# Optimization experiments

Hardware: AMD Instinct MI355X
Metric: run time of the kernel (lower is better)

## Reference

```python
import jax, jax.numpy as jnp
import numpy as np

D = 1024
H = 16
HD = D // H


def setup_inputs() -> dict:
    key = jax.random.key(0)
    ks = jax.random.split(key, 12)
    s = 0.02
    return {
        "X": jax.random.normal(ks[0], (8, 1024, D), dtype=jnp.float32),
        "W_qkv": jax.random.normal(ks[1], (D, 3 * D), dtype=jnp.float32) * s,
        "b_qkv": jnp.zeros((3 * D,), dtype=jnp.float32),
        "W_out": jax.random.normal(ks[2], (D, D), dtype=jnp.float32) * s,
        "b_out": jnp.zeros((D,), dtype=jnp.float32),
        "ln1_g": jnp.ones((D,), dtype=jnp.float32),
        "ln1_b": jnp.zeros((D,), dtype=jnp.float32),
        "ln2_g": jnp.ones((D,), dtype=jnp.float32),
        "ln2_b": jnp.zeros((D,), dtype=jnp.float32),
        "W_ff1": jax.random.normal(ks[3], (D, 4 * D), dtype=jnp.float32) * s,
        "b_ff1": jnp.zeros((4 * D,), dtype=jnp.float32),
        "W_ff2": jax.random.normal(ks[4], (4 * D, D), dtype=jnp.float32) * s,
        "b_ff2": jnp.zeros((D,), dtype=jnp.float32),
    }


def _layer_norm(x, g, b, eps=1e-5):
    mu = jnp.mean(x, axis=-1, keepdims=True)
    var = jnp.var(x, axis=-1, keepdims=True)
    return (x - mu) * jax.lax.rsqrt(var + eps) * g + b


def reference(X, W_qkv, b_qkv, W_out, b_out, ln1_g, ln1_b, ln2_g, ln2_b,
              W_ff1, b_ff1, W_ff2, b_ff2):
    B, T, _ = X.shape
    qkv = X @ W_qkv + b_qkv                      # [B,T,3D]
    qkv = qkv.reshape(B, T, 3, H, HD).transpose(2, 0, 3, 1, 4)  # [3,B,H,T,hd]
    Q, K, V = qkv[0], qkv[1], qkv[2]
    scores = jnp.einsum("bhqd,bhkd->bhqk", Q, K) / np.sqrt(HD).astype(np.float32)
    attn = jax.nn.softmax(scores, axis=-1)
    ctx = jnp.einsum("bhqk,bhkd->bhqd", attn, V)  # [B,H,T,hd]
    ctx = ctx.transpose(0, 2, 1, 3).reshape(B, T, D)
    attn_out = ctx @ W_out + b_out
    X1 = _layer_norm(attn_out + X, ln1_g, ln1_b)
    ffn = jax.nn.gelu(X1 @ W_ff1 + b_ff1, approximate=False) @ W_ff2 + b_ff2
    return _layer_norm(ffn + X1, ln2_g, ln2_b)
```

## Files before the change

kernel.cpp:

```cpp
#include <hip/hip_runtime.h>
#include <hip/hip_bf16.h>
#include <cstdint>

typedef unsigned short u16;
typedef __bf16 bf16x8 __attribute__((ext_vector_type(8)));
typedef float f32x4 __attribute__((ext_vector_type(4)));

__device__ __forceinline__ u16 f2bf(float f) {
  unsigned int u = __float_as_uint(f);
  u += 0x7FFFu + ((u >> 16) & 1u);
  return (u16)(u >> 16);
}
__device__ __forceinline__ unsigned int pack2(float a, float b) {
  return (unsigned int)f2bf(a) | ((unsigned int)f2bf(b) << 16);
}

__global__ __launch_bounds__(256) void cast_bf16_k(const float* __restrict__ in,
                                                   u16* __restrict__ out) {
  const int i = (blockIdx.x * 256 + threadIdx.x) * 4;
  const float4 v = *(const float4*)(in + i);
  uint2 p;
  p.x = pack2(v.x, v.y);
  p.y = pack2(v.z, v.w);
  *(uint2*)(out + i) = p;
}

__global__ __launch_bounds__(256) void transpose_cast_k(const float* __restrict__ in,
                                                        u16* __restrict__ out,
                                                        int R, int C) {
  __shared__ float tile[32][33];
  const int bx = blockIdx.x * 32, by = blockIdx.y * 32;
  const int tx = threadIdx.x & 31, ty = threadIdx.x >> 5;
#pragma unroll
  for (int i = 0; i < 32; i += 8)
    tile[ty + i][tx] = in[(size_t)(by + ty + i) * C + (bx + tx)];
  __syncthreads();
#pragma unroll
  for (int i = 0; i < 32; i += 8)
    out[(size_t)(bx + ty + i) * R + (by + tx)] = f2bf(tile[tx][ty + i]);
}

template <int EPI>
__device__ __forceinline__ void epi_store(float v, int row, int col, int N,
                                          const float* __restrict__ resid,
                                          float* __restrict__ out_f,
                                          u16* __restrict__ out_b,
                                          u16* __restrict__ q_out,
                                          u16* __restrict__ k_out,
                                          u16* __restrict__ vt_out) {
  if (EPI == 0) {
    const int which = col >> 10, rem = col & 1023;
    const int h = rem >> 6, d = rem & 63;
    const int b = row >> 10, tq = row & 1023;
    const size_t bh = (size_t)(b * 16 + h);
    const u16 u = f2bf(v);
    if (which == 0)
      q_out[(bh * 1024 + tq) * 64 + d] = u;
    else if (which == 1)
      k_out[(bh * 1024 + tq) * 64 + d] = u;
    else
      vt_out[(bh * 64 + d) * 1024 + tq] = u;
  } else if (EPI == 1) {
    out_f[(size_t)row * N + col] = v + resid[(size_t)row * N + col];
  } else {
    const float gl = 0.5f * v * (1.0f + erff(v * 0.70710678118f));
    out_b[(size_t)row * N + col] = f2bf(gl);
  }
}

#define SYNC_PRE                                      \
  __builtin_amdgcn_s_barrier();                       \
  asm volatile("s_waitcnt lgkmcnt(0)" ::: "memory");  \
  __builtin_amdgcn_sched_barrier(0);                  \
  __builtin_amdgcn_s_setprio(1);

#define SYNC_POST                                     \
  __builtin_amdgcn_s_setprio(0);                      \
  __builtin_amdgcn_sched_barrier(0);                  \
  __builtin_amdgcn_s_barrier();

template <int EPI>
__global__ __launch_bounds__(512, 2) void gemm8(
    const u16* __restrict__ A, const u16* __restrict__ Bt,
    const float* __restrict__ bias, const float* __restrict__ resid,
    float* __restrict__ out_f, u16* __restrict__ out_b,
    u16* __restrict__ q_out, u16* __restrict__ k_out, u16* __restrict__ vt_out,
    int M, int N, int K) {
  __shared__ char lds[131072];
  const int tid = threadIdx.x;
  const int wave = tid >> 6, lane = tid & 63;
  const int llo = lane & 15, lhi = lane >> 4;
  const int wm = wave >> 2, wn = wave & 3;
  const int NT = K >> 6;
  const int nbx = N >> 8;
  const int cpx = gridDim.x >> 3;
  const int wg = (blockIdx.x & 7) * cpx + (blockIdx.x >> 3);
  const int m0 = (wg / nbx) << 8, n0 = (wg % nbx) << 8;

  const int rloc = tid >> 3;
  const int scol = (((tid & 7) * 16) ^ ((rloc & 7) << 4)) >> 1;
  const int swz = (llo & 7) << 4;

  f32x4 acc[8][4] = {};
  bf16x8 aF[2][4][2], bF[2][2][2];

#define STAGE_A(tt, hi)                                                         \
  if ((tt) < NT) {                                                              \
    char* db_ = lds + (((tt) & 1) << 16);                                       \
    _Pragma("unroll") for (int c_ = 0; c_ < 2; ++c_) {                          \
      const u16* g_ =                                                           \
          A + (size_t)(m0 + (hi) * 128 + c_ * 64 + rloc) * K + (tt) * 64 + scol;\
      __builtin_amdgcn_global_load_lds(                                         \
          (const __attribute__((address_space(1))) unsigned int*)g_,            \
          (__attribute__((address_space(3))) unsigned int*)(db_ + (hi) * 16384 +\
                                                           c_ * 8192 + wave * 1024), \
          16, 0, 0);                                                            \
    }                                                                           \
  }

#define STAGE_B(tt, hi)                                                         \
  if ((tt) < NT) {                                                              \
    char* db_ = lds + (((tt) & 1) << 16) + 32768;                               \
    _Pragma("unroll") for (int c_ = 0; c_ < 2; ++c_) {                          \
      const u16* g_ =                                                           \
          Bt + (size_t)(n0 + (hi) * 128 + c_ * 64 + rloc) * K + (tt) * 64 + scol;\
      __builtin_amdgcn_global_load_lds(                                         \
          (const __attribute__((address_space(1))) unsigned int*)g_,            \
          (__attribute__((address_space(3))) unsigned int*)(db_ + (hi) * 16384 +\
                                                           c_ * 8192 + wave * 1024), \
          16, 0, 0);                                                            \
    }                                                                           \
  }

#define LOAD_A(mh)                                                              \
  _Pragma("unroll") for (int mq_ = 0; mq_ < 4; ++mq_)                           \
  _Pragma("unroll") for (int kk_ = 0; kk_ < 2; ++kk_)                           \
    aF[mh][mq_][kk_] = *(const bf16x8*)(ldsA + (wm * 128 + (mh) * 64 + mq_ * 16 + llo) * 128 + \
                                        ((kk_ * 64 + lhi * 16) ^ swz));

#define LOAD_B(nh)                                                              \
  _Pragma("unroll") for (int nf_ = 0; nf_ < 2; ++nf_)                           \
  _Pragma("unroll") for (int kk_ = 0; kk_ < 2; ++kk_)                           \
    bF[nh][nf_][kk_] = *(const bf16x8*)(ldsB + (wn * 64 + (nh) * 32 + nf_ * 16 + llo) * 128 + \
                                        ((kk_ * 64 + lhi * 16) ^ swz));

#define DO_MFMA(mh, nh)                                                         \
  _Pragma("unroll") for (int mq_ = 0; mq_ < 4; ++mq_)                           \
  _Pragma("unroll") for (int nf_ = 0; nf_ < 2; ++nf_)                           \
  _Pragma("unroll") for (int kk_ = 0; kk_ < 2; ++kk_)                           \
    acc[(mh) * 4 + mq_][(nh) * 2 + nf_] = __builtin_amdgcn_mfma_f32_16x16x32_bf16( \
        aF[mh][mq_][kk_], bF[nh][nf_][kk_], acc[(mh) * 4 + mq_][(nh) * 2 + nf_], 0, 0, 0);

  STAGE_A(0, 0) STAGE_A(0, 1) STAGE_B(0, 0) STAGE_B(0, 1) STAGE_A(1, 0) STAGE_A(1, 1)
  asm volatile("s_waitcnt vmcnt(4)" ::: "memory");
  __builtin_amdgcn_s_barrier();

  for (int t = 0; t < NT; ++t) {
    const char* ldsA = lds + ((t & 1) << 16);
    const char* ldsB = ldsA + 32768;
    LOAD_A(0) LOAD_B(0)
    STAGE_B(t + 1, 0)
    SYNC_PRE DO_MFMA(0, 0) SYNC_POST
    LOAD_A(1)
    STAGE_B(t + 1, 1)
    SYNC_PRE DO_MFMA(1, 0) SYNC_POST
    LOAD_B(1)
    STAGE_A(t + 2, 0)
    SYNC_PRE DO_MFMA(0, 1) SYNC_POST
    STAGE_A(t + 2, 1)
    asm volatile("s_waitcnt vmcnt(4)" ::: "memory");
    SYNC_PRE DO_MFMA(1, 1) SYNC_POST
  }

#pragma unroll
  for (int mf = 0; mf < 8; ++mf) {
#pragma unroll
    for (int nf = 0; nf < 4; ++nf) {
      const int col = n0 + wn * 64 + nf * 16 + llo;
      const int rowb = m0 + wm * 128 + mf * 16 + lhi * 4;
      const float bv = bias[col];
#pragma unroll
      for (int r = 0; r < 4; ++r)
        epi_store<EPI>(acc[mf][nf][r] + bv, rowb + r, col, N, resid, out_f, out_b,
                       q_out, k_out, vt_out);
    }
  }
#undef STAGE_A
#undef STAGE_B
#undef LOAD_A
#undef LOAD_B
#undef DO_MFMA
}

template <int EPI>
__global__ __launch_bounds__(512, 2) void gemm8n(
    const u16* __restrict__ A, const u16* __restrict__ Bt,
    const float* __restrict__ bias, const float* __restrict__ resid,
    float* __restrict__ out_f, u16* __restrict__ out_b,
    u16* __restrict__ q_out, u16* __restrict__ k_out, u16* __restrict__ vt_out,
    int M, int N, int K) {
  __shared__ char lds[98304];
  const int tid = threadIdx.x;
  const int wave = tid >> 6, lane = tid & 63;
  const int llo = lane & 15, lhi = lane >> 4;
  const int wm = wave >> 1, wn = wave & 1;
  const int NT = K >> 6;
  const int nbx = N >> 7;
  const int cpx = gridDim.x >> 3;
  const int wg = (blockIdx.x & 7) * cpx + (blockIdx.x >> 3);
  const int m0 = (wg / nbx) << 8, n0 = (wg % nbx) << 7;

  const int rloc = tid >> 3;
  const int scol = (((tid & 7) * 16) ^ ((rloc & 7) << 4)) >> 1;
  const int swz = (llo & 7) << 4;

  f32x4 acc[4][4] = {};
  bf16x8 aF[2][2][2], bF[2][2][2];

#define STAGE_A(tt, hi)                                                         \
  if ((tt) < NT) {                                                              \
    char* db_ = lds + ((tt) & 1) * 49152;                                       \
    _Pragma("unroll") for (int c_ = 0; c_ < 2; ++c_) {                          \
      const u16* g_ =                                                           \
          A + (size_t)(m0 + (hi) * 128 + c_ * 64 + rloc) * K + (tt) * 64 + scol;\
      __builtin_amdgcn_global_load_lds(                                         \
          (const __attribute__((address_space(1))) unsigned int*)g_,            \
          (__attribute__((address_space(3))) unsigned int*)(db_ + (hi) * 16384 +\
                                                           c_ * 8192 + wave * 1024), \
          16, 0, 0);                                                            \
    }                                                                           \
  }

#define STAGE_B(tt)                                                             \
  if ((tt) < NT) {                                                              \
    char* db_ = lds + ((tt) & 1) * 49152 + 32768;                               \
    _Pragma("unroll") for (int c_ = 0; c_ < 2; ++c_) {                          \
      const u16* g_ =                                                           \
          Bt + (size_t)(n0 + c_ * 64 + rloc) * K + (tt) * 64 + scol;            \
      __builtin_amdgcn_global_load_lds(                                         \
          (const __attribute__((address_space(1))) unsigned int*)g_,            \
          (__attribute__((address_space(3))) unsigned int*)(db_ +               \
                                                           c_ * 8192 + wave * 1024), \
          16, 0, 0);                                                            \
    }                                                                           \
  }

#define LOAD_A(mh)                                                              \
  _Pragma("unroll") for (int mf_ = 0; mf_ < 2; ++mf_)                           \
  _Pragma("unroll") for (int kk_ = 0; kk_ < 2; ++kk_)                           \
    aF[mh][mf_][kk_] = *(const bf16x8*)(ldsA + (wm * 64 + (mh) * 32 + mf_ * 16 + llo) * 128 + \
                                        ((kk_ * 64 + lhi * 16) ^ swz));

#define LOAD_B(nh)                                                              \
  _Pragma("unroll") for (int nf_ = 0; nf_ < 2; ++nf_)                           \
  _Pragma("unroll") for (int kk_ = 0; kk_ < 2; ++kk_)                           \
    bF[nh][nf_][kk_] = *(const bf16x8*)(ldsB + (wn * 64 + (nh) * 32 + nf_ * 16 + llo) * 128 + \
                                        ((kk_ * 64 + lhi * 16) ^ swz));

#define DO_MFMA(mh, nh)                                                         \
  _Pragma("unroll") for (int mf_ = 0; mf_ < 2; ++mf_)                           \
  _Pragma("unroll") for (int nf_ = 0; nf_ < 2; ++nf_)                           \
  _Pragma("unroll") for (int kk_ = 0; kk_ < 2; ++kk_)                           \
    acc[(mh) * 2 + mf_][(nh) * 2 + nf_] = __builtin_amdgcn_mfma_f32_16x16x32_bf16( \
        aF[mh][mf_][kk_], bF[nh][nf_][kk_], acc[(mh) * 2 + mf_][(nh) * 2 + nf_], 0, 0, 0);

  STAGE_A(0, 0) STAGE_A(0, 1) STAGE_B(0) STAGE_A(1, 0) STAGE_A(1, 1)
  asm volatile("s_waitcnt vmcnt(4)" ::: "memory");
  __builtin_amdgcn_s_barrier();

  for (int t = 0; t < NT; ++t) {
    const char* ldsA = lds + (t & 1) * 49152;
    const char* ldsB = ldsA + 32768;
    LOAD_A(0) LOAD_B(0)
    STAGE_B(t + 1)
    SYNC_PRE DO_MFMA(0, 0) SYNC_POST
    LOAD_A(1)
    STAGE_A(t + 2, 0)
    SYNC_PRE DO_MFMA(1, 0) SYNC_POST
    LOAD_B(1)
    STAGE_A(t + 2, 1)
    SYNC_PRE DO_MFMA(0, 1) SYNC_POST
    asm volatile("s_waitcnt vmcnt(4)" ::: "memory");
    SYNC_PRE DO_MFMA(1, 1) SYNC_POST
  }

#pragma unroll
  for (int mf = 0; mf < 4; ++mf) {
#pragma unroll
    for (int nf = 0; nf < 4; ++nf) {
      const int col = n0 + wn * 64 + nf * 16 + llo;
      const int rowb = m0 + wm * 64 + mf * 16 + lhi * 4;
      const float bv = bias[col];
#pragma unroll
      for (int r = 0; r < 4; ++r)
        epi_store<EPI>(acc[mf][nf][r] + bv, rowb + r, col, N, resid, out_f, out_b,
                       q_out, k_out, vt_out);
    }
  }
#undef STAGE_A
#undef STAGE_B
#undef LOAD_A
#undef LOAD_B
#undef DO_MFMA
}

__global__ __launch_bounds__(256) void attn_flash_k(const u16* __restrict__ Qb,
                                                    const u16* __restrict__ Kb,
                                                    const u16* __restrict__ Vt,
                                                    u16* __restrict__ ctx) {
  __shared__ char lds[8192 + 8192 + 4 * 2048];
  char* Ks = lds;
  char* Vs = lds + 8192;
  const int tid = threadIdx.x;
  const int wave = tid >> 6, lane = tid & 63;
  const int llo = lane & 15, lhi = lane >> 4;
  char* Ps = lds + 16384 + wave * 2048;
  const int bh = blockIdx.y;
  const int q0 = blockIdx.x * 64 + wave * 16;
  const size_t hq = (size_t)bh * 1024 * 64;
  const int swz = (llo & 7) << 4;

  const u16* qrow = Qb + hq + (size_t)(q0 + llo) * 64;
  const bf16x8 qf0 = *(const bf16x8*)(qrow + lhi * 8);
  const bf16x8 qf1 = *(const bf16x8*)(qrow + 32 + lhi * 8);

  f32x4 O[4] = {};
  float m = -3.0e38f, l = 0.f;
  const float C = 0.18033688011112042f;

  for (int t = 0; t < 16; ++t) {
    const int kv0 = t * 64;
    __syncthreads();
#pragma unroll
    for (int j = 0; j < 2; ++j) {
      const int p = (j * 256 + tid) * 16;
      const int r = p >> 7;
      const int c = (p & 127) ^ ((r & 7) << 4);
      const u16* gk = Kb + hq + (size_t)(kv0 + r) * 64 + (c >> 1);
      __builtin_amdgcn_global_load_lds(
          (const __attribute__((address_space(1))) unsigned int*)gk,
          (__attribute__((address_space(3))) unsigned int*)(Ks + (j * 256 + wave * 64) * 16),
          16, 0, 0);
      const u16* gv = Vt + (size_t)bh * 64 * 1024 + (size_t)r * 1024 + kv0 + (c >> 1);
      __builtin_amdgcn_global_load_lds(
          (const __attribute__((address_space(1))) unsigned int*)gv,
          (__attribute__((address_space(3))) unsigned int*)(Vs + (j * 256 + wave * 64) * 16),
          16, 0, 0);
    }
    __syncthreads();

    f32x4 s[4];
#pragma unroll
    for (int kt = 0; kt < 4; ++kt) {
      const int row = kt * 16 + llo;
      const bf16x8 k0 = *(const bf16x8*)(Ks + row * 128 + ((lhi * 16) ^ swz));
      const bf16x8 k1 = *(const bf16x8*)(Ks + row * 128 + ((64 + lhi * 16) ^ swz));
      f32x4 a = {};
      a = __builtin_amdgcn_mfma_f32_16x16x32_bf16(k0, qf0, a, 0, 0, 0);
      a = __builtin_amdgcn_mfma_f32_16x16x32_bf16(k1, qf1, a, 0, 0, 0);
      s[kt] = a;
    }

    float tmax = -3.0e38f;
#pragma unroll
    for (int kt = 0; kt < 4; ++kt)
#pragma unroll
      for (int r = 0; r < 4; ++r) tmax = fmaxf(tmax, s[kt][r]);
    tmax = fmaxf(tmax, __shfl_xor(tmax, 16));
    tmax = fmaxf(tmax, __shfl_xor(tmax, 32));
    const float mnew = fmaxf(m, tmax);
    const float sc = exp2f((m - mnew) * C);
    float tsum = 0.f;
#pragma unroll
    for (int kt = 0; kt < 4; ++kt)
#pragma unroll
      for (int r = 0; r < 4; ++r) {
        const float pv = exp2f((s[kt][r] - mnew) * C);
        s[kt][r] = pv;
        tsum += pv;
      }
    tsum += __shfl_xor(tsum, 16);
    tsum += __shfl_xor(tsum, 32);
    l = l * sc + tsum;
    m = mnew;
#pragma unroll
    for (int dt = 0; dt < 4; ++dt) O[dt] *= sc;

#pragma unroll
    for (int kt = 0; kt < 4; ++kt) {
      uint2 pk;
      pk.x = pack2(s[kt][0], s[kt][1]);
      pk.y = pack2(s[kt][2], s[kt][3]);
      *(uint2*)(Ps + llo * 128 + ((kt * 32 + lhi * 8) ^ swz)) = pk;
    }
    bf16x8 pb[2];
#pragma unroll
    for (int kc = 0; kc < 2; ++kc)
      pb[kc] = *(const bf16x8*)(Ps + llo * 128 + ((kc * 64 + lhi * 16) ^ swz));

#pragma unroll
    for (int dt = 0; dt < 4; ++dt) {
      const int vrow = dt * 16 + llo;
#pragma unroll
      for (int kc = 0; kc < 2; ++kc) {
        const bf16x8 vf = *(const bf16x8*)(Vs + vrow * 128 + ((kc * 64 + lhi * 16) ^ swz));
        O[dt] = __builtin_amdgcn_mfma_f32_16x16x32_bf16(vf, pb[kc], O[dt], 0, 0, 0);
      }
    }
  }

  const float inv = 1.0f / l;
  const int b = bh >> 4, h = bh & 15;
  u16* crow = ctx + ((size_t)(b * 1024 + q0 + llo)) * 1024 + h * 64;
#pragma unroll
  for (int dt = 0; dt < 4; ++dt) {
    uint2 pk;
    pk.x = pack2(O[dt][0] * inv, O[dt][1] * inv);
    pk.y = pack2(O[dt][2] * inv, O[dt][3] * inv);
    *(uint2*)(crow + dt * 16 + lhi * 4) = pk;
  }
}

__global__ __launch_bounds__(256) void layernorm_k(const float* __restrict__ y,
                                                   const float* __restrict__ g,
                                                   const float* __restrict__ be,
                                                   u16* __restrict__ out_b,
                                                   float* __restrict__ out_f) {
  const int row = blockIdx.x;
  const int t = threadIdx.x;
  const float* yr = y + (size_t)row * 1024;
  const float4 v = *(const float4*)(yr + t * 4);
  float s = v.x + v.y + v.z + v.w;
  float s2 = v.x * v.x + v.y * v.y + v.z * v.z + v.w * v.w;
#pragma unroll
  for (int m = 1; m < 64; m <<= 1) {
    s += __shfl_xor(s, m);
    s2 += __shfl_xor(s2, m);
  }
  __shared__ float red[8];
  const int wv = t >> 6, lane = t & 63;
  if (lane == 0) {
    red[wv * 2] = s;
    red[wv * 2 + 1] = s2;
  }
  __syncthreads();
  s = red[0] + red[2] + red[4] + red[6];
  s2 = red[1] + red[3] + red[5] + red[7];
  const float mu = s * (1.0f / 1024.0f);
  const float var = s2 * (1.0f / 1024.0f) - mu * mu;
  const float inv = rsqrtf(var + 1e-5f);
  const int c = t * 4;
  const float4 gg = *(const float4*)(g + c);
  const float4 bb = *(const float4*)(be + c);
  const float o0 = (v.x - mu) * inv * gg.x + bb.x;
  const float o1 = (v.y - mu) * inv * gg.y + bb.y;
  const float o2 = (v.z - mu) * inv * gg.z + bb.z;
  const float o3 = (v.w - mu) * inv * gg.w + bb.w;
  if (out_f) {
    float4 o = {o0, o1, o2, o3};
    *(float4*)(out_f + (size_t)row * 1024 + c) = o;
  }
  if (out_b) {
    uint2 p;
    p.x = pack2(o0, o1);
    p.y = pack2(o2, o3);
    *(uint2*)(out_b + (size_t)row * 1024 + c) = p;
  }
}

extern "C" void kernel_launch(void* const* d_in, const int* in_sizes, int n_in,
                              void* d_out, int out_size, void* d_ws, size_t ws_size,
                              hipStream_t stream) {
  const float* X = (const float*)d_in[0];
  const float* W_qkv = (const float*)d_in[1];
  const float* b_qkv = (const float*)d_in[2];
  const float* W_out = (const float*)d_in[3];
  const float* b_out = (const float*)d_in[4];
  const float* ln1_g = (const float*)d_in[5];
  const float* ln1_b = (const float*)d_in[6];
  const float* ln2_g = (const float*)d_in[7];
  const float* ln2_b = (const float*)d_in[8];
  const float* W_ff1 = (const float*)d_in[9];
  const float* b_ff1 = (const float*)d_in[10];
  const float* W_ff2 = (const float*)d_in[11];
  const float* b_ff2 = (const float*)d_in[12];

  char* ws = (char*)d_ws;
  size_t off = 0;
  auto alloc = [&](size_t bytes) {
    char* p = ws + off;
    off += (bytes + 255) & ~(size_t)255;
    return p;
  };
  u16* Xb = (u16*)alloc(8192ull * 1024 * 2);
  u16* Wqkvt = (u16*)alloc(3072ull * 1024 * 2);
  u16* Woutt = (u16*)alloc(1024ull * 1024 * 2);
  u16* Wff1t = (u16*)alloc(4096ull * 1024 * 2);
  u16* Wff2t = (u16*)alloc(1024ull * 4096 * 2);
  u16* Qb = (u16*)alloc(128ull * 1024 * 64 * 2);
  u16* Kb = (u16*)alloc(128ull * 1024 * 64 * 2);
  u16* Vtb = (u16*)alloc(128ull * 1024 * 64 * 2);
  u16* ctx = (u16*)alloc(8192ull * 1024 * 2);
  float* y1 = (float*)alloc(8192ull * 1024 * 4);
  u16* X1b = (u16*)alloc(8192ull * 1024 * 2);
  float* X1f = (float*)alloc(8192ull * 1024 * 4);
  u16* hbuf = Qb;

  cast_bf16_k<<<8192, 256, 0, stream>>>(X, Xb);
  transpose_cast_k<<<dim3(96, 32), 256, 0, stream>>>(W_qkv, Wqkvt, 1024, 3072);
  transpose_cast_k<<<dim3(32, 32), 256, 0, stream>>>(W_out, Woutt, 1024, 1024);
  transpose_cast_k<<<dim3(128, 32), 256, 0, stream>>>(W_ff1, Wff1t, 1024, 4096);
  transpose_cast_k<<<dim3(32, 128), 256, 0, stream>>>(W_ff2, Wff2t, 4096, 1024);

  gemm8n<0><<<768, 512, 0, stream>>>(Xb, Wqkvt, b_qkv, nullptr, nullptr, nullptr,
                                     Qb, Kb, Vtb, 8192, 3072, 1024);
  attn_flash_k<<<dim3(16, 128), 256, 0, stream>>>(Qb, Kb, Vtb, ctx);
  gemm8n<1><<<256, 512, 0, stream>>>(ctx, Woutt, b_out, X, y1, nullptr,
                                     nullptr, nullptr, nullptr, 8192, 1024, 1024);
  layernorm_k<<<8192, 256, 0, stream>>>(y1, ln1_g, ln1_b, X1b, X1f);
  gemm8<2><<<512, 512, 0, stream>>>(X1b, Wff1t, b_ff1, nullptr, nullptr, hbuf,
                                    nullptr, nullptr, nullptr, 8192, 4096, 1024);
  gemm8n<1><<<256, 512, 0, stream>>>(hbuf, Wff2t, b_ff2, X1f, y1, nullptr,
                                     nullptr, nullptr, nullptr, 8192, 1024, 4096);
  layernorm_k<<<8192, 256, 0, stream>>>(y1, ln2_g, ln2_b, nullptr, (float*)d_out);
}
```

Before: 532.0 us.

## Prefetch B tiles two steps ahead in GEMMs; load attention K/V directly from global

Both GEMM kernels now stage B tiles two iterations ahead, matching the A tiles, and raise the vmcnt wait thresholds to match, giving a deeper and more uniform prefetch. The attention kernel drops the cooperative K/V staging into LDS and its two block-wide barriers per tile. Each wave instead loads its K and V fragments straight from global memory into registers, relying on cache for reuse across waves. The trade is more global/L2 traffic and register pressure in attention, and more outstanding loads in the GEMMs, in exchange for fewer barriers.

```diff
diff --git a/kernel.cpp b/kernel.cpp
--- a/kernel.cpp
+++ b/kernel.cpp
@@ -151,24 +151,25 @@
     acc[(mh) * 4 + mq_][(nh) * 2 + nf_] = __builtin_amdgcn_mfma_f32_16x16x32_bf16( \
         aF[mh][mq_][kk_], bF[nh][nf_][kk_], acc[(mh) * 4 + mq_][(nh) * 2 + nf_], 0, 0, 0);
 
-  STAGE_A(0, 0) STAGE_A(0, 1) STAGE_B(0, 0) STAGE_B(0, 1) STAGE_A(1, 0) STAGE_A(1, 1)
-  asm volatile("s_waitcnt vmcnt(4)" ::: "memory");
+  STAGE_A(0, 0) STAGE_A(0, 1) STAGE_B(0, 0) STAGE_B(0, 1)
+  STAGE_A(1, 0) STAGE_A(1, 1) STAGE_B(1, 0) STAGE_B(1, 1)
+  asm volatile("s_waitcnt vmcnt(8)" ::: "memory");
   __builtin_amdgcn_s_barrier();
 
   for (int t = 0; t < NT; ++t) {
     const char* ldsA = lds + ((t & 1) << 16);
     const char* ldsB = ldsA + 32768;
     LOAD_A(0) LOAD_B(0)
-    STAGE_B(t + 1, 0)
     SYNC_PRE DO_MFMA(0, 0) SYNC_POST
     LOAD_A(1)
-    STAGE_B(t + 1, 1)
     SYNC_PRE DO_MFMA(1, 0) SYNC_POST
     LOAD_B(1)
     STAGE_A(t + 2, 0)
+    STAGE_A(t + 2, 1)
     SYNC_PRE DO_MFMA(0, 1) SYNC_POST
-    STAGE_A(t + 2, 1)
-    asm volatile("s_waitcnt vmcnt(4)" ::: "memory");
+    STAGE_B(t + 2, 0)
+    STAGE_B(t + 2, 1)
+    asm volatile("s_waitcnt vmcnt(8)" ::: "memory");
     SYNC_PRE DO_MFMA(1, 1) SYNC_POST
   }
 
@@ -264,23 +265,24 @@
     acc[(mh) * 2 + mf_][(nh) * 2 + nf_] = __builtin_amdgcn_mfma_f32_16x16x32_bf16( \
         aF[mh][mf_][kk_], bF[nh][nf_][kk_], acc[(mh) * 2 + mf_][(nh) * 2 + nf_], 0, 0, 0);
 
-  STAGE_A(0, 0) STAGE_A(0, 1) STAGE_B(0) STAGE_A(1, 0) STAGE_A(1, 1)
-  asm volatile("s_waitcnt vmcnt(4)" ::: "memory");
+  STAGE_A(0, 0) STAGE_A(0, 1) STAGE_B(0)
+  STAGE_A(1, 0) STAGE_A(1, 1) STAGE_B(1)
+  asm volatile("s_waitcnt vmcnt(6)" ::: "memory");
   __builtin_amdgcn_s_barrier();
 
   for (int t = 0; t < NT; ++t) {
     const char* ldsA = lds + (t & 1) * 49152;
     const char* ldsB = ldsA + 32768;
     LOAD_A(0) LOAD_B(0)
-    STAGE_B(t + 1)
     SYNC_PRE DO_MFMA(0, 0) SYNC_POST
     LOAD_A(1)
-    STAGE_A(t + 2, 0)
     SYNC_PRE DO_MFMA(1, 0) SYNC_POST
     LOAD_B(1)
+    STAGE_A(t + 2, 0)
     STAGE_A(t + 2, 1)
     SYNC_PRE DO_MFMA(0, 1) SYNC_POST
-    asm volatile("s_waitcnt vmcnt(4)" ::: "memory");
+    STAGE_B(t + 2)
+    asm volatile("s_waitcnt vmcnt(6)" ::: "memory");
     SYNC_PRE DO_MFMA(1, 1) SYNC_POST
   }
 
@@ -304,17 +306,15 @@
 #undef DO_MFMA
 }
 
-__global__ __launch_bounds__(256) void attn_flash_k(const u16* __restrict__ Qb,
-                                                    const u16* __restrict__ Kb,
-                                                    const u16* __restrict__ Vt,
-                                                    u16* __restrict__ ctx) {
-  __shared__ char lds[8192 + 8192 + 4 * 2048];
-  char* Ks = lds;
-  char* Vs = lds + 8192;
+__global__ __launch_bounds__(256) void attn_flash2_k(const u16* __restrict__ Qb,
+                                                     const u16* __restrict__ Kb,
+                                                     const u16* __restrict__ Vt,
+                                                     u16* __restrict__ ctx) {
+  __shared__ char Ps_all[4 * 2048];
   const int tid = threadIdx.x;
   const int wave = tid >> 6, lane = tid & 63;
   const int llo = lane & 15, lhi = lane >> 4;
-  char* Ps = lds + 16384 + wave * 2048;
+  char* Ps = Ps_all + wave * 2048;
   const int bh = blockIdx.y;
   const int q0 = blockIdx.x * 64 + wave * 16;
   const size_t hq = (size_t)bh * 1024 * 64;
@@ -324,42 +324,34 @@
   const bf16x8 qf0 = *(const bf16x8*)(qrow + lhi * 8);
   const bf16x8 qf1 = *(const bf16x8*)(qrow + 32 + lhi * 8);
 
+  const u16* kbase = Kb + hq + (size_t)llo * 64 + lhi * 8;
+  const u16* vbase = Vt + (size_t)bh * 64 * 1024 + (size_t)llo * 1024 + lhi * 8;
+
   f32x4 O[4] = {};
   float m = -3.0e38f, l = 0.f;
   const float C = 0.18033688011112042f;
 
   for (int t = 0; t < 16; ++t) {
     const int kv0 = t * 64;
-    __syncthreads();
-#pragma unroll
-    for (int j = 0; j < 2; ++j) {
-      const int p = (j * 256 + tid) * 16;
-      const int r = p >> 7;
-      const int c = (p & 127) ^ ((r & 7) << 4);
-      const u16* gk = Kb + hq + (size_t)(kv0 + r) * 64 + (c >> 1);
-      __builtin_amdgcn_global_load_lds(
-          (const __attribute__((address_space(1))) unsigned int*)gk,
-          (__attribute__((address_space(3))) unsigned int*)(Ks + (j * 256 + wave * 64) * 16),
-          16, 0, 0);
-      const u16* gv = Vt + (size_t)bh * 64 * 1024 + (size_t)r * 1024 + kv0 + (c >> 1);
-      __builtin_amdgcn_global_load_lds(
-          (const __attribute__((address_space(1))) unsigned int*)gv,
-          (__attribute__((address_space(3))) unsigned int*)(Vs + (j * 256 + wave * 64) * 16),
-          16, 0, 0);
-    }
-    __syncthreads();
 
     f32x4 s[4];
 #pragma unroll
     for (int kt = 0; kt < 4; ++kt) {
-      const int row = kt * 16 + llo;
-      const bf16x8 k0 = *(const bf16x8*)(Ks + row * 128 + ((lhi * 16) ^ swz));
-      const bf16x8 k1 = *(const bf16x8*)(Ks + row * 128 + ((64 + lhi * 16) ^ swz));
+      const u16* kr = kbase + (size_t)(kv0 + kt * 16) * 64;
+      const bf16x8 k0 = *(const bf16x8*)(kr);
+      const bf16x8 k1 = *(const bf16x8*)(kr + 32);
       f32x4 a = {};
       a = __builtin_amdgcn_mfma_f32_16x16x32_bf16(k0, qf0, a, 0, 0, 0);
       a = __builtin_amdgcn_mfma_f32_16x16x32_bf16(k1, qf1, a, 0, 0, 0);
       s[kt] = a;
     }
+
+    bf16x8 vf[4][2];
+#pragma unroll
+    for (int dt = 0; dt < 4; ++dt)
+#pragma unroll
+      for (int kc = 0; kc < 2; ++kc)
+        vf[dt][kc] = *(const bf16x8*)(vbase + (size_t)(dt * 16) * 1024 + kv0 + kc * 32);
 
     float tmax = -3.0e38f;
 #pragma unroll
@@ -399,14 +391,10 @@
       pb[kc] = *(const bf16x8*)(Ps + llo * 128 + ((kc * 64 + lhi * 16) ^ swz));
 
 #pragma unroll
-    for (int dt = 0; dt < 4; ++dt) {
-      const int vrow = dt * 16 + llo;
-#pragma unroll
-      for (int kc = 0; kc < 2; ++kc) {
-        const bf16x8 vf = *(const bf16x8*)(Vs + vrow * 128 + ((kc * 64 + lhi * 16) ^ swz));
-        O[dt] = __builtin_amdgcn_mfma_f32_16x16x32_bf16(vf, pb[kc], O[dt], 0, 0, 0);
-      }
-    }
+    for (int dt = 0; dt < 4; ++dt)
+#pragma unroll
+      for (int kc = 0; kc < 2; ++kc)
+        O[dt] = __builtin_amdgcn_mfma_f32_16x16x32_bf16(vf[dt][kc], pb[kc], O[dt], 0, 0, 0);
   }
 
   const float inv = 1.0f / l;
@@ -514,7 +502,7 @@
 
   gemm8n<0><<<768, 512, 0, stream>>>(Xb, Wqkvt, b_qkv, nullptr, nullptr, nullptr,
                                      Qb, Kb, Vtb, 8192, 3072, 1024);
-  attn_flash_k<<<dim3(16, 128), 256, 0, stream>>>(Qb, Kb, Vtb, ctx);
+  attn_flash2_k<<<dim3(16, 128), 256, 0, stream>>>(Qb, Kb, Vtb, ctx);
   gemm8n<1><<<256, 512, 0, stream>>>(ctx, Woutt, b_out, X, y1, nullptr,
                                      nullptr, nullptr, nullptr, 8192, 1024, 1024);
   layernorm_k<<<8192, 256, 0, stream>>>(y1, ln1_g, ln1_b, X1b, X1f);
```

Result: slower. 680.8 us (+28.0%).
